# Kernel tuning notes

Measured on AMD Instinct MI355X. Metric: run time of the kernel, lower is better.

## Reference

```python
import jax, jax.numpy as jnp
import numpy as np

C, U, V, D, B = 5, 6144, 6144, 64, 4096  # classes, users, items, feat dim, batch pairs


def setup_inputs() -> dict:
    key = jax.random.key(0)
    ks = jax.random.split(key, 16)
    s = 1.0 / np.sqrt(D)
    adj = (jax.random.uniform(ks[0], (C, U, V)) < 0.01).astype(jnp.float32)
    return {
        "u": jax.random.randint(ks[1], (B,), 0, U),
        "v": jax.random.randint(ks[2], (B,), 0, V),
        "u_emb": jax.random.normal(ks[3], (U, D), jnp.float32) * 0.1,
        "v_emb": jax.random.normal(ks[4], (V, D), jnp.float32) * 0.1,
        "W1u": jax.random.normal(ks[5], (C, D, D), jnp.float32) * s,
        "b1u": jnp.zeros((C, D), jnp.float32),
        "W1v": jax.random.normal(ks[6], (C, D, D), jnp.float32) * s,
        "b1v": jnp.zeros((C, D), jnp.float32),
        "W2u": jax.random.normal(ks[7], (C, D, D), jnp.float32) * s,
        "b2u": jnp.zeros((C, D), jnp.float32),
        "W2v": jax.random.normal(ks[8], (C, D, D), jnp.float32) * s,
        "b2v": jnp.zeros((C, D), jnp.float32),
        "Q": jax.random.normal(ks[9], (C, D, D), jnp.float32) * s,
        "adj": adj,
    }


def reference(u, v, u_emb, v_emb, W1u, b1u, W1v, b1v, W2u, b2u, W2v, b2v, Q, adj):
    # ---- layer 1: per-class graph convolution, summed over rating classes ----
    # user codes aggregate item features through adj_c; item codes through adj_c^T
    msg_v = jnp.einsum("vd,cde->cve", v_emb, W1v)            # [C,V,D]
    h_u = jax.nn.relu(jnp.einsum("cuv,cve->ue", adj, msg_v) + b1v.sum(0))  # [U,D]
    msg_u = jnp.einsum("ud,cde->cue", u_emb, W1u)            # [C,U,D]
    h_v = jax.nn.relu(jnp.einsum("cuv,cue->ve", adj, msg_u) + b1u.sum(0))  # [V,D]
    # ---- layer 2 ----
    z_u = jnp.einsum("cuv,cve->ue", adj, jnp.einsum("vd,cde->cve", h_v, W2u)) + b2u.sum(0)
    z_v = jnp.einsum("cuv,cue->ve", adj, jnp.einsum("ud,cde->cue", h_u, W2v)) + b2v.sum(0)
    # ---- bilinear decoder over batch of (user, item) pairs ----
    zu = z_u[u]                                              # [B,D] gather
    zv = z_v[v]                                              # [B,D] gather
    logits = jnp.einsum("bd,cde,be->bc", zu, Q, zv)          # [B,C] per-class rating logits
    return logits
```

## Files before the change

### kernel.cpp

```cpp
#include <hip/hip_runtime.h>

#define NC   5
#define NU   6144
#define NV   6144
#define ND   64
#define NB   4096
#define CAP  128
#define NW   192

__device__ __forceinline__ unsigned int spread4(unsigned int x) {
  x &= 0xFFu;
  x = (x | (x << 12)) & 0x000F000Fu;
  x = (x | (x << 6))  & 0x03030303u;
  x = (x | (x << 3))  & 0x11111111u;
  return x;
}

__global__ __launch_bounds__(256) void k_bitmask(
    const float* __restrict__ adj,
    unsigned int* __restrict__ rowmask,
    unsigned int* __restrict__ colmask) {
  __shared__ unsigned int rowwords[64][8];
  const int b = blockIdx.x;
  const int c  = b / 2304;
  const int rem = b - c * 2304;
  const int tu = rem / 24;
  const int tv = rem - tu * 24;
  const int wave = threadIdx.x >> 6;
  const int lane = threadIdx.x & 63;

  float4 av[16];
  {
    const float* base = adj +
        ((size_t)(c * NU + tu * 64 + wave * 16) * NV + tv * 256);
    #pragma unroll
    for (int rr = 0; rr < 16; ++rr)
      av[rr] = ((const float4*)(base + (size_t)rr * NV))[lane];
  }
  #pragma unroll
  for (int rr = 0; rr < 16; ++rr) {
    const unsigned long long b0 = __ballot(av[rr].x != 0.0f);
    const unsigned long long b1 = __ballot(av[rr].y != 0.0f);
    const unsigned long long b2 = __ballot(av[rr].z != 0.0f);
    const unsigned long long b3 = __ballot(av[rr].w != 0.0f);
    if (lane < 8) {
      const unsigned int e0 = spread4((unsigned int)(b0 >> (lane * 8)));
      const unsigned int e1 = spread4((unsigned int)(b1 >> (lane * 8)));
      const unsigned int e2 = spread4((unsigned int)(b2 >> (lane * 8)));
      const unsigned int e3 = spread4((unsigned int)(b3 >> (lane * 8)));
      rowwords[wave * 16 + rr][lane] = e0 | (e1 << 1) | (e2 << 2) | (e3 << 3);
    }
  }
  __syncthreads();

  {
    const int r2 = threadIdx.x >> 2;
    const int k  = threadIdx.x & 3;
    uint2 w;
    w.x = rowwords[r2][k * 2 + 0];
    w.y = rowwords[r2][k * 2 + 1];
    *(uint2*)(rowmask + (size_t)(c * NU + tu * 64 + r2) * NW + tv * 8 + k * 2) = w;
  }

  {
    const int j = threadIdx.x;
    const int w = j >> 5, bit = j & 31;
    unsigned int w0 = 0, w1 = 0;
    #pragma unroll
    for (int r = 0; r < 32; ++r) {
      w0 |= ((rowwords[r][w]      >> bit) & 1u) << r;
      w1 |= ((rowwords[r + 32][w] >> bit) & 1u) << r;
    }
    uint2 ww; ww.x = w0; ww.y = w1;
    *(uint2*)(colmask + (size_t)(c * NV + tv * 256 + j) * NW + tu * 2) = ww;
  }
}

__global__ __launch_bounds__(256) void k_expand(
    const unsigned int* __restrict__ mask,
    int* __restrict__ cnt,
    unsigned short* __restrict__ idx) {
  const int wave = threadIdx.x >> 6;
  const int lane = threadIdx.x & 63;
  const int R = blockIdx.x * 4 + wave;
  const unsigned int* mrow = mask + (size_t)R * NW;
  const unsigned int w0 = mrow[lane];
  const unsigned int w1 = mrow[lane + 64];
  const unsigned int w2 = mrow[lane + 128];
  const int t0 = __popc(w0), t1 = __popc(w1), t2 = __popc(w2);
  int p0 = t0, p1 = t1, p2 = t2;
  #pragma unroll
  for (int d = 1; d < 64; d <<= 1) {
    const int y0 = __shfl_up(p0, d, 64);
    const int y1 = __shfl_up(p1, d, 64);
    const int y2 = __shfl_up(p2, d, 64);
    if (lane >= d) { p0 += y0; p1 += y1; p2 += y2; }
  }
  const int T0 = __shfl(p0, 63, 64);
  const int T1 = __shfl(p1, 63, 64);
  const int T2 = __shfl(p2, 63, 64);
  if (lane == 0) cnt[R] = T0 + T1 + T2;
  unsigned short* orow = idx + (size_t)R * CAP;
  int e0 = p0 - t0;
  int e1 = T0 + p1 - t1;
  int e2 = T0 + T1 + p2 - t2;
  unsigned int m;
  m = w0;
  while (m) { int bb = __ffs(m) - 1; if (e0 < CAP) orow[e0] = (unsigned short)(lane * 32 + bb); ++e0; m &= m - 1; }
  m = w1;
  while (m) { int bb = __ffs(m) - 1; if (e1 < CAP) orow[e1] = (unsigned short)((lane + 64) * 32 + bb); ++e1; m &= m - 1; }
  m = w2;
  while (m) { int bb = __ffs(m) - 1; if (e2 < CAP) orow[e2] = (unsigned short)((lane + 128) * 32 + bb); ++e2; m &= m - 1; }
}

__global__ __launch_bounds__(256) void k_gather(
    const int* __restrict__ cnt,
    const unsigned short* __restrict__ idx,
    const float* __restrict__ table,
    float* __restrict__ agg) {
  __shared__ float4 red4[4][16];
  const int wave = threadIdx.x >> 6;
  const int lane = threadIdx.x & 63;
  const int R = blockIdx.x * 4 + wave;
  const int g    = lane >> 4;
  const int e16  = lane & 15;
  int n = cnt[R];
  n = n > CAP ? CAP : n;
  const unsigned short* l = idx + (size_t)R * CAP;
  const float4* tab = (const float4*)table;
  float4 a0 = make_float4(0.f,0.f,0.f,0.f), a1 = a0, a2 = a0, a3 = a0;
  int i = 0;
  for (; i + 16 <= n; i += 16) {
    const int j0 = l[i + g], j1 = l[i + 4 + g];
    const int j2 = l[i + 8 + g], j3 = l[i + 12 + g];
    const float4 x0 = tab[j0 * 16 + e16];
    const float4 x1 = tab[j1 * 16 + e16];
    const float4 x2 = tab[j2 * 16 + e16];
    const float4 x3 = tab[j3 * 16 + e16];
    a0.x += x0.x; a0.y += x0.y; a0.z += x0.z; a0.w += x0.w;
    a1.x += x1.x; a1.y += x1.y; a1.z += x1.z; a1.w += x1.w;
    a2.x += x2.x; a2.y += x2.y; a2.z += x2.z; a2.w += x2.w;
    a3.x += x3.x; a3.y += x3.y; a3.z += x3.z; a3.w += x3.w;
  }
  for (; i + 4 <= n; i += 4) {
    const float4 x = tab[(int)l[i + g] * 16 + e16];
    a0.x += x.x; a0.y += x.y; a0.z += x.z; a0.w += x.w;
  }
  if (i + g < n) {
    const float4 x = tab[(int)l[i + g] * 16 + e16];
    a1.x += x.x; a1.y += x.y; a1.z += x.z; a1.w += x.w;
  }
  a0.x += a1.x + a2.x + a3.x;
  a0.y += a1.y + a2.y + a3.y;
  a0.z += a1.z + a2.z + a3.z;
  a0.w += a1.w + a2.w + a3.w;
  #pragma unroll
  for (int off = 16; off < 64; off <<= 1) {
    a0.x += __shfl_xor(a0.x, off, 64);
    a0.y += __shfl_xor(a0.y, off, 64);
    a0.z += __shfl_xor(a0.z, off, 64);
    a0.w += __shfl_xor(a0.w, off, 64);
  }
  if (g == 0) red4[wave][e16] = a0;
  __syncthreads();
  if (g == 0) ((float4*)agg)[(size_t)R * 16 + e16] = red4[wave][e16];
}

__global__ __launch_bounds__(256) void k_gemm5(
    const float* __restrict__ agg,
    const float* __restrict__ W,
    const float* __restrict__ bias,
    float* __restrict__ out,
    int M, int do_relu) {
  const int lane = threadIdx.x & 63;
  const int wave = threadIdx.x >> 6;
  const int r0 = blockIdx.x * 16 + wave * 4;
  float bs = 0.0f;
  #pragma unroll
  for (int c = 0; c < NC; ++c) bs += bias[c * 64 + lane];
  float acc[4] = {bs, bs, bs, bs};
  for (int c = 0; c < NC; ++c) {
    float w[64];
    #pragma unroll
    for (int d = 0; d < 64; ++d) w[d] = W[c * 4096 + d * 64 + lane];
    #pragma unroll
    for (int r = 0; r < 4; ++r) {
      const float4* ar = (const float4*)(agg + ((size_t)c * M + r0 + r) * 64);
      #pragma unroll
      for (int d4 = 0; d4 < 16; ++d4) {
        const float4 a = ar[d4];
        acc[r] = fmaf(a.x, w[d4 * 4 + 0], acc[r]);
        acc[r] = fmaf(a.y, w[d4 * 4 + 1], acc[r]);
        acc[r] = fmaf(a.z, w[d4 * 4 + 2], acc[r]);
        acc[r] = fmaf(a.w, w[d4 * 4 + 3], acc[r]);
      }
    }
  }
  #pragma unroll
  for (int r = 0; r < 4; ++r) {
    const float x = do_relu ? fmaxf(acc[r], 0.0f) : acc[r];
    out[(size_t)(r0 + r) * 64 + lane] = x;
  }
}

__global__ __launch_bounds__(256) void k_decoder(
    const int* __restrict__ uu, const int* __restrict__ vv,
    const float* __restrict__ z_u, const float* __restrict__ z_v,
    const float* __restrict__ Q,
    float* __restrict__ out) {
  const int lane = threadIdx.x & 63;
  const int wave = threadIdx.x >> 6;
  const int b = blockIdx.x * 4 + wave;
  const int ub = uu[b];
  const int vb = vv[b];
  const float zve = z_v[(size_t)vb * 64 + lane];
  const float* zu = z_u + (size_t)ub * 64;
  #pragma unroll
  for (int c = 0; c < NC; ++c) {
    const float* Qc = Q + c * 64 * 64;
    float t = 0.0f;
    #pragma unroll
    for (int d = 0; d < 64; ++d) t = fmaf(zu[d], Qc[d * 64 + lane], t);
    float p = t * zve;
    #pragma unroll
    for (int off = 32; off > 0; off >>= 1) p += __shfl_xor(p, off, 64);
    if (lane == 0) out[(size_t)b * NC + c] = p;
  }
}

extern "C" void kernel_launch(void* const* d_in, const int* in_sizes, int n_in,
                              void* d_out, int out_size, void* d_ws, size_t ws_size,
                              hipStream_t stream) {
  const int*   u     = (const int*)d_in[0];
  const int*   v     = (const int*)d_in[1];
  const float* u_emb = (const float*)d_in[2];
  const float* v_emb = (const float*)d_in[3];
  const float* W1u   = (const float*)d_in[4];
  const float* b1u   = (const float*)d_in[5];
  const float* W1v   = (const float*)d_in[6];
  const float* b1v   = (const float*)d_in[7];
  const float* W2u   = (const float*)d_in[8];
  const float* b2u   = (const float*)d_in[9];
  const float* W2v   = (const float*)d_in[10];
  const float* b2v   = (const float*)d_in[11];
  const float* Q     = (const float*)d_in[12];
  const float* adj   = (const float*)d_in[13];
  float* out = (float*)d_out;

  char* ws = (char*)d_ws;
  int* csr_cnt = (int*)ws;
  int* csc_cnt = csr_cnt + NC * NU;
  unsigned short* csr_idx = (unsigned short*)(ws + 245760);
  unsigned short* csc_idx = (unsigned short*)(ws + 245760 + 7864320);
  char* maskbase = ws + 245760 + 2 * 7864320;
  unsigned int* rowmask = (unsigned int*)maskbase;
  unsigned int* colmask = (unsigned int*)(maskbase + 23592960);
  float* aggA = (float*)maskbase;
  float* aggB = (float*)(maskbase + 7864320);
  float* h_u  = (float*)(maskbase + 15728640);
  float* h_v  = (float*)(maskbase + 17301504);
  float* z_u  = (float*)(maskbase + 18874368);
  float* z_v  = (float*)(maskbase + 20447232);

  k_bitmask<<<5 * 96 * 24, 256, 0, stream>>>(adj, rowmask, colmask);
  k_expand<<<NC * NU / 4, 256, 0, stream>>>(rowmask, csr_cnt, csr_idx);
  k_expand<<<NC * NV / 4, 256, 0, stream>>>(colmask, csc_cnt, csc_idx);

  k_gather<<<NC * NU / 4, 256, 0, stream>>>(csr_cnt, csr_idx, v_emb, aggA);
  k_gather<<<NC * NV / 4, 256, 0, stream>>>(csc_cnt, csc_idx, u_emb, aggB);
  k_gemm5<<<NU / 16, 256, 0, stream>>>(aggA, W1v, b1v, h_u, NU, 1);
  k_gemm5<<<NV / 16, 256, 0, stream>>>(aggB, W1u, b1u, h_v, NV, 1);
  k_gather<<<NC * NU / 4, 256, 0, stream>>>(csr_cnt, csr_idx, h_v, aggA);
  k_gather<<<NC * NV / 4, 256, 0, stream>>>(csc_cnt, csc_idx, h_u, aggB);
  k_gemm5<<<NU / 16, 256, 0, stream>>>(aggA, W2u, b2u, z_u, NU, 0);
  k_gemm5<<<NV / 16, 256, 0, stream>>>(aggB, W2v, b2v, z_v, NV, 0);
  k_decoder<<<NB / 4, 256, 0, stream>>>(u, v, z_u, z_v, Q, out);
}
```

Baseline: 1.263 ms.

## Transpose bitmask layout for per-lane row expansion and merge paired kernel launches

```diff
diff --git a/kernel.cpp b/kernel.cpp
--- a/kernel.cpp
+++ b/kernel.cpp
@@ -7,6 +7,7 @@
 #define NB   4096
 #define CAP  128
 #define NW   192
+#define HALF (NC * NU)
 
 __device__ __forceinline__ unsigned int spread4(unsigned int x) {
   x &= 0xFFu;
@@ -18,9 +19,8 @@
 
 __global__ __launch_bounds__(256) void k_bitmask(
     const float* __restrict__ adj,
-    unsigned int* __restrict__ rowmask,
-    unsigned int* __restrict__ colmask) {
-  __shared__ unsigned int rowwords[64][8];
+    unsigned int* __restrict__ maskT) {
+  __shared__ unsigned int rowwords[64][9];
   const int b = blockIdx.x;
   const int c  = b / 2304;
   const int rem = b - c * 2304;
@@ -54,12 +54,11 @@
   __syncthreads();
 
   {
-    const int r2 = threadIdx.x >> 2;
-    const int k  = threadIdx.x & 3;
-    uint2 w;
-    w.x = rowwords[r2][k * 2 + 0];
-    w.y = rowwords[r2][k * 2 + 1];
-    *(uint2*)(rowmask + (size_t)(c * NU + tu * 64 + r2) * NW + tv * 8 + k * 2) = w;
+    const int k  = threadIdx.x >> 5;
+    const int rb = threadIdx.x & 31;
+    unsigned int* p = maskT + ((size_t)c * 192 + tv * 8 + k) * 6144 + tu * 64;
+    p[rb]      = rowwords[rb][k];
+    p[rb + 32] = rowwords[rb + 32][k];
   }
 
   {
@@ -71,52 +70,51 @@
       w0 |= ((rowwords[r][w]      >> bit) & 1u) << r;
       w1 |= ((rowwords[r + 32][w] >> bit) & 1u) << r;
     }
-    uint2 ww; ww.x = w0; ww.y = w1;
-    *(uint2*)(colmask + (size_t)(c * NV + tv * 256 + j) * NW + tu * 2) = ww;
+    unsigned int* p = maskT +
+        ((size_t)(NC + c) * 192 + tu * 2) * 6144 + tv * 256 + j;
+    p[0]    = w0;
+    p[6144] = w1;
   }
 }
 
 __global__ __launch_bounds__(256) void k_expand(
-    const unsigned int* __restrict__ mask,
+    const unsigned int* __restrict__ maskT,
     int* __restrict__ cnt,
     unsigned short* __restrict__ idx) {
-  const int wave = threadIdx.x >> 6;
-  const int lane = threadIdx.x & 63;
-  const int R = blockIdx.x * 4 + wave;
-  const unsigned int* mrow = mask + (size_t)R * NW;
-  const unsigned int w0 = mrow[lane];
-  const unsigned int w1 = mrow[lane + 64];
-  const unsigned int w2 = mrow[lane + 128];
-  const int t0 = __popc(w0), t1 = __popc(w1), t2 = __popc(w2);
-  int p0 = t0, p1 = t1, p2 = t2;
-  #pragma unroll
-  for (int d = 1; d < 64; d <<= 1) {
-    const int y0 = __shfl_up(p0, d, 64);
-    const int y1 = __shfl_up(p1, d, 64);
-    const int y2 = __shfl_up(p2, d, 64);
-    if (lane >= d) { p0 += y0; p1 += y1; p2 += y2; }
-  }
-  const int T0 = __shfl(p0, 63, 64);
-  const int T1 = __shfl(p1, 63, 64);
-  const int T2 = __shfl(p2, 63, 64);
-  if (lane == 0) cnt[R] = T0 + T1 + T2;
+  const int wv = blockIdx.x * 4 + (threadIdx.x >> 6);
+  const int lane = threadIdx.x & 63;
+  const int sc = wv / 96;
+  const int g  = wv - sc * 96;
+  const int dim = g * 64 + lane;
+  const unsigned int* base = maskT + (size_t)sc * 192 * 6144 + dim;
+  const int R = sc * 6144 + dim;
   unsigned short* orow = idx + (size_t)R * CAP;
-  int e0 = p0 - t0;
-  int e1 = T0 + p1 - t1;
-  int e2 = T0 + T1 + p2 - t2;
-  unsigned int m;
-  m = w0;
-  while (m) { int bb = __ffs(m) - 1; if (e0 < CAP) orow[e0] = (unsigned short)(lane * 32 + bb); ++e0; m &= m - 1; }
-  m = w1;
-  while (m) { int bb = __ffs(m) - 1; if (e1 < CAP) orow[e1] = (unsigned short)((lane + 64) * 32 + bb); ++e1; m &= m - 1; }
-  m = w2;
-  while (m) { int bb = __ffs(m) - 1; if (e2 < CAP) orow[e2] = (unsigned short)((lane + 128) * 32 + bb); ++e2; m &= m - 1; }
+  int cur = 0;
+  for (int wb = 0; wb < NW; wb += 16) {
+    unsigned int wreg[16];
+    #pragma unroll
+    for (int t = 0; t < 16; ++t)
+      wreg[t] = base[(size_t)(wb + t) * 6144];
+    #pragma unroll
+    for (int t = 0; t < 16; ++t) {
+      unsigned int m = wreg[t];
+      const int wbase = (wb + t) * 32;
+      while (m) {
+        const int bb = __ffs(m) - 1;
+        if (cur < CAP) orow[cur] = (unsigned short)(wbase + bb);
+        ++cur;
+        m &= m - 1;
+      }
+    }
+  }
+  cnt[R] = cur < CAP ? cur : CAP;
 }
 
 __global__ __launch_bounds__(256) void k_gather(
     const int* __restrict__ cnt,
     const unsigned short* __restrict__ idx,
-    const float* __restrict__ table,
+    const float* __restrict__ tabA,
+    const float* __restrict__ tabB,
     float* __restrict__ agg) {
   __shared__ float4 red4[4][16];
   const int wave = threadIdx.x >> 6;
@@ -127,7 +125,7 @@
   int n = cnt[R];
   n = n > CAP ? CAP : n;
   const unsigned short* l = idx + (size_t)R * CAP;
-  const float4* tab = (const float4*)table;
+  const float4* tab = (const float4*)(R < HALF ? tabA : tabB);
   float4 a0 = make_float4(0.f,0.f,0.f,0.f), a1 = a0, a2 = a0, a3 = a0;
   int i = 0;
   for (; i + 16 <= n; i += 16) {
@@ -168,13 +166,19 @@
 
 __global__ __launch_bounds__(256) void k_gemm5(
     const float* __restrict__ agg,
-    const float* __restrict__ W,
-    const float* __restrict__ bias,
-    float* __restrict__ out,
-    int M, int do_relu) {
-  const int lane = threadIdx.x & 63;
-  const int wave = threadIdx.x >> 6;
-  const int r0 = blockIdx.x * 16 + wave * 4;
+    const float* __restrict__ Wa, const float* __restrict__ ba,
+    float* __restrict__ outA,
+    const float* __restrict__ Wb, const float* __restrict__ bb,
+    float* __restrict__ outB,
+    int do_relu) {
+  const int half = blockIdx.x >= 384;
+  const float* W    = half ? Wb : Wa;
+  const float* bias = half ? bb : ba;
+  float* out        = half ? outB : outA;
+  const float* aggh = agg + (size_t)half * HALF * 64;
+  const int lane = threadIdx.x & 63;
+  const int wave = threadIdx.x >> 6;
+  const int r0 = (blockIdx.x - half * 384) * 16 + wave * 4;
   float bs = 0.0f;
   #pragma unroll
   for (int c = 0; c < NC; ++c) bs += bias[c * 64 + lane];
@@ -185,7 +189,7 @@
     for (int d = 0; d < 64; ++d) w[d] = W[c * 4096 + d * 64 + lane];
     #pragma unroll
     for (int r = 0; r < 4; ++r) {
-      const float4* ar = (const float4*)(agg + ((size_t)c * M + r0 + r) * 64);
+      const float4* ar = (const float4*)(aggh + ((size_t)c * 6144 + r0 + r) * 64);
       #pragma unroll
       for (int d4 = 0; d4 < 16; ++d4) {
         const float4 a = ar[d4];
@@ -248,31 +252,22 @@
   float* out = (float*)d_out;
 
   char* ws = (char*)d_ws;
-  int* csr_cnt = (int*)ws;
-  int* csc_cnt = csr_cnt + NC * NU;
-  unsigned short* csr_idx = (unsigned short*)(ws + 245760);
-  unsigned short* csc_idx = (unsigned short*)(ws + 245760 + 7864320);
-  char* maskbase = ws + 245760 + 2 * 7864320;
-  unsigned int* rowmask = (unsigned int*)maskbase;
-  unsigned int* colmask = (unsigned int*)(maskbase + 23592960);
-  float* aggA = (float*)maskbase;
-  float* aggB = (float*)(maskbase + 7864320);
-  float* h_u  = (float*)(maskbase + 15728640);
-  float* h_v  = (float*)(maskbase + 17301504);
-  float* z_u  = (float*)(maskbase + 18874368);
-  float* z_v  = (float*)(maskbase + 20447232);
-
-  k_bitmask<<<5 * 96 * 24, 256, 0, stream>>>(adj, rowmask, colmask);
-  k_expand<<<NC * NU / 4, 256, 0, stream>>>(rowmask, csr_cnt, csr_idx);
-  k_expand<<<NC * NV / 4, 256, 0, stream>>>(colmask, csc_cnt, csc_idx);
-
-  k_gather<<<NC * NU / 4, 256, 0, stream>>>(csr_cnt, csr_idx, v_emb, aggA);
-  k_gather<<<NC * NV / 4, 256, 0, stream>>>(csc_cnt, csc_idx, u_emb, aggB);
-  k_gemm5<<<NU / 16, 256, 0, stream>>>(aggA, W1v, b1v, h_u, NU, 1);
-  k_gemm5<<<NV / 16, 256, 0, stream>>>(aggB, W1u, b1u, h_v, NV, 1);
-  k_gather<<<NC * NU / 4, 256, 0, stream>>>(csr_cnt, csr_idx, h_v, aggA);
-  k_gather<<<NC * NV / 4, 256, 0, stream>>>(csc_cnt, csc_idx, h_u, aggB);
-  k_gemm5<<<NU / 16, 256, 0, stream>>>(aggA, W2u, b2u, z_u, NU, 0);
-  k_gemm5<<<NV / 16, 256, 0, stream>>>(aggB, W2v, b2v, z_v, NV, 0);
+  int* cnt = (int*)ws;
+  unsigned short* idxL = (unsigned short*)(ws + 245760);
+  char* maskbase = ws + 245760 + 15728640;
+  unsigned int* maskT = (unsigned int*)maskbase;
+  float* agg = (float*)maskbase;
+  float* h_u = (float*)(maskbase + 15728640);
+  float* h_v = (float*)(maskbase + 17301504);
+  float* z_u = (float*)(maskbase + 18874368);
+  float* z_v = (float*)(maskbase + 20447232);
+
+  k_bitmask<<<NC * 96 * 24, 256, 0, stream>>>(adj, maskT);
+  k_expand<<<240, 256, 0, stream>>>(maskT, cnt, idxL);
+
+  k_gather<<<2 * HALF / 4, 256, 0, stream>>>(cnt, idxL, v_emb, u_emb, agg);
+  k_gemm5<<<768, 256, 0, stream>>>(agg, W1v, b1v, h_u, W1u, b1u, h_v, 1);
+  k_gather<<<2 * HALF / 4, 256, 0, stream>>>(cnt, idxL, h_v, h_u, agg);
+  k_gemm5<<<768, 256, 0, stream>>>(agg, W2u, b2u, z_u, W2v, b2v, z_v, 0);
   k_decoder<<<NB / 4, 256, 0, stream>>>(u, v, z_u, z_v, Q, out);
 }
```

Result: faster. 1.232 ms (-2.4%).
